# Kernel tuning notes

Measured on AMD Instinct MI355X. Metric: run time of the kernel, lower is better.

## Reference

```python
import jax, jax.numpy as jnp
import numpy as np

B, S, DIM = 4, 2048, 512
HEADS, DHEAD = 8, 64
INNER = HEADS * DHEAD


def setup_inputs() -> dict:
    key = jax.random.key(0)
    k1, k2, k3, k4 = jax.random.split(key, 4)
    x = jax.random.normal(k1, (B, S, DIM), dtype=jnp.float32)
    W_qkv = jax.random.normal(k2, (DIM, 3 * INNER), dtype=jnp.float32) * (DIM ** -0.5)
    W_out = jax.random.normal(k3, (INNER, DIM), dtype=jnp.float32) * (INNER ** -0.5)
    b_out = jnp.zeros((DIM,), dtype=jnp.float32)
    # learnable log-temperature, initialized to log(dim_head**-0.5)
    log_temp = jnp.asarray(np.log(DHEAD ** -0.5), dtype=jnp.float32)
    return {"x": x, "W_qkv": W_qkv, "log_temp": log_temp, "W_out": W_out, "b_out": b_out}


def reference(x, W_qkv, log_temp, W_out, b_out):
    b, s, _ = x.shape
    qkv = x @ W_qkv  # [b, s, 3*inner]
    q, k, v = jnp.split(qkv, 3, axis=-1)
    # [b, s, inner] -> [b, h, s, d]
    reshape = lambda t: t.reshape(b, s, HEADS, DHEAD).transpose(0, 2, 1, 3)
    q, k, v = reshape(q), reshape(k), reshape(v)
    dots = jnp.einsum("bhid,bhjd->bhij", q, k) * jnp.exp(log_temp)
    mask_value = -jnp.finfo(dots.dtype).max
    eye = jnp.eye(s, dtype=bool)
    dots = jnp.where(eye, mask_value, dots)
    attn = jax.nn.softmax(dots, axis=-1)
    out = jnp.einsum("bhij,bhjd->bhid", attn, v)
    out = out.transpose(0, 2, 1, 3).reshape(b, s, INNER)
    return out @ W_out + b_out
```

## Files before the change

kernel.cpp:

```cpp
#include <hip/hip_runtime.h>
#include <hip/hip_bf16.h>

#define BB 4
#define SS 2048
#define DIMM 512
#define HH 8
#define DD 64
#define NQKV 1536

typedef float  floatx4 __attribute__((ext_vector_type(4)));
typedef short  bf16x8  __attribute__((ext_vector_type(8)));
typedef short  bf16x4  __attribute__((ext_vector_type(4)));

#define MFMA16(A, B, C) __builtin_amdgcn_mfma_f32_16x16x32_bf16(A, B, C, 0, 0, 0)

__device__ __forceinline__ unsigned short f2bf(float f) {
    unsigned int u = __float_as_uint(f);
    u += 0x7FFFu + ((u >> 16) & 1u);
    return (unsigned short)(u >> 16);
}

__device__ __forceinline__ unsigned int f2bf_pk(float lo, float hi) {
    float2 f; f.x = lo; f.y = hi;
    __hip_bfloat162 h = __float22bfloat162_rn(f);
    return *reinterpret_cast<unsigned int*>(&h);
}

__device__ __forceinline__ float fast_exp2(float x) {
#if __has_builtin(__builtin_amdgcn_exp2f)
    return __builtin_amdgcn_exp2f(x);
#else
    return __exp2f(x);
#endif
}

__device__ __forceinline__ void gl_lds16(const void* g, void* l) {
    __builtin_amdgcn_global_load_lds(
        (__attribute__((address_space(1))) void*)g,
        (__attribute__((address_space(3))) void*)l,
        16, 0, 0);
}

__global__ __launch_bounds__(256) void k_prep(
    const float* __restrict__ x, const float* __restrict__ W_qkv,
    const float* __restrict__ W_out,
    unsigned short* __restrict__ xb, unsigned short* __restrict__ Wq_t,
    unsigned short* __restrict__ Wo_t) {
    __shared__ float t[32][33];
    int bid = blockIdx.x, tid = threadIdx.x;
    if (bid < 4096) {
        int i = (bid * 256 + tid) * 4;
        float4 v = *(const float4*)(x + i);
        ushort4 o;
        o.x = f2bf(v.x); o.y = f2bf(v.y); o.z = f2bf(v.z); o.w = f2bf(v.w);
        *(ushort4*)(xb + i) = o;
        return;
    }
    const float* in; unsigned short* out; int R = 512, C, bx, by;
    if (bid < 4864) { in = W_qkv; out = Wq_t; C = 1536; int blk = bid - 4096; bx = blk % 48; by = blk / 48; }
    else            { in = W_out; out = Wo_t; C = 512;  int blk = bid - 4864; bx = blk % 16; by = blk / 16; }
    int tx = tid & 31, ty = tid >> 5;
    int c0 = bx * 32, r0 = by * 32;
    for (int i = 0; i < 4; i++) {
        int r = r0 + ty + i * 8;
        t[ty + i * 8][tx] = in[(size_t)r * C + c0 + tx];
    }
    __syncthreads();
    for (int i = 0; i < 4; i++) {
        int cc = c0 + ty + i * 8;
        out[(size_t)cc * R + r0 + tx] = f2bf(t[tx][ty + i * 8]);
    }
}

__global__ __launch_bounds__(256) void k_gemm_qkv(
    const unsigned short* __restrict__ A,
    const unsigned short* __restrict__ Bt,
    const float* __restrict__ log_temp,
    unsigned short* __restrict__ Qb,
    unsigned short* __restrict__ Kb,
    unsigned short* __restrict__ Vt) {
    __shared__ unsigned short smem[2][128 * 64];
    unsigned short* As = smem[0];
    unsigned short* Bs = smem[1];
    const int K = 512;
    int m0 = blockIdx.x * 128, n0 = blockIdx.y * 128;
    int tid = threadIdx.x;
    int w = tid >> 6, lane = tid & 63;
    int c = lane & 15, q4 = lane >> 4;
    int wm = w >> 1, wn = w & 1;
    float qscale = __expf(log_temp[0]) * 1.44269504f;

    floatx4 acc[4][4] = {};

    for (int k0 = 0; k0 < K; k0 += 64) {
        __syncthreads();
        for (int i = 0; i < 4; i++) {
            int cidx = w * 256 + i * 64 + lane;
            int row = cidx >> 3, cc = cidx & 7;
            int gcc = cc ^ (row & 7);
            gl_lds16(A + (size_t)(m0 + row) * K + k0 + gcc * 8,
                     As + (size_t)(w * 256 + i * 64) * 8);
            gl_lds16(Bt + (size_t)(n0 + row) * K + k0 + gcc * 8,
                     Bs + (size_t)(w * 256 + i * 64) * 8);
        }
        __syncthreads();
        bf16x8 aF[2][4], bF[2][4];
        for (int kh = 0; kh < 2; kh++)
            for (int mt = 0; mt < 4; mt++) {
                int row = wm * 64 + mt * 16 + c;
                aF[kh][mt] = *(const bf16x8*)&As[row * 64 + (((kh * 4 + q4) ^ (row & 7)) * 8)];
            }
        for (int kh = 0; kh < 2; kh++)
            for (int nt = 0; nt < 4; nt++) {
                int row = wn * 64 + nt * 16 + c;
                bF[kh][nt] = *(const bf16x8*)&Bs[row * 64 + (((kh * 4 + q4) ^ (row & 7)) * 8)];
            }
        for (int kh = 0; kh < 2; kh++)
            for (int mt = 0; mt < 4; mt++)
                for (int nt = 0; nt < 4; nt++)
                    acc[mt][nt] = MFMA16(aF[kh][mt], bF[kh][nt], acc[mt][nt]);
    }

    if (n0 < 1024) {
        for (int nt = 0; nt < 4; nt++) {
            int n = n0 + wn * 64 + nt * 16 + c;
            int t = n >> 9, inner = n & 511;
            int h = inner >> 6, d = inner & 63;
            for (int mt = 0; mt < 4; mt++) {
                for (int r = 0; r < 4; r++) {
                    int m = m0 + wm * 64 + mt * 16 + q4 * 4 + r;
                    int b = m >> 11, s = m & 2047;
                    int bh = b * 8 + h;
                    float v = acc[mt][nt][r];
                    if (t == 0)  Qb[((size_t)bh * SS + s) * 64 + d] = f2bf(v * qscale);
                    else         Kb[((size_t)bh * SS + s) * 64 + d] = f2bf(v);
                }
            }
        }
    } else {
        unsigned short* T = &smem[0][0];
        int b = m0 >> 11, s_base = m0 & 2047;
        for (int half = 0; half < 2; half++) {
            __syncthreads();
            if (wn == half) {
                for (int nt = 0; nt < 4; nt++)
                    for (int mt = 0; mt < 4; mt++)
                        for (int r = 0; r < 4; r++)
                            T[(nt * 16 + c) * 136 + wm * 64 + mt * 16 + q4 * 4 + r] =
                                f2bf(acc[mt][nt][r]);
            }
            __syncthreads();
            for (int rr = 0; rr < 4; rr++) {
                int nl = w * 16 + rr * 4 + q4;
                int ml = c * 8;
                bf16x8 v = *(const bf16x8*)&T[nl * 136 + ml];
                int n = n0 + half * 64 + nl;
                int h = (n >> 6) - 16, d = n & 63;
                int bh = b * 8 + h;
                *(bf16x8*)(Vt + ((size_t)bh * 64 + d) * SS + s_base + ml) = v;
            }
        }
    }
}

__global__ __launch_bounds__(256, 4) void k_attn(
    const unsigned short* __restrict__ Qb,
    const unsigned short* __restrict__ Kb,
    const unsigned short* __restrict__ Vt,
    unsigned short* __restrict__ AO) {
    __shared__ unsigned short Ks[2][64 * 64];
    __shared__ unsigned short Vs[2][64 * 64];
    int q0 = blockIdx.x * 128;
    int h = blockIdx.y, b = blockIdx.z;
    int bh = b * 8 + h;
    int tid = threadIdx.x, w = tid >> 6, lane = tid & 63;
    int c = lane & 15, q4 = lane >> 4;

    const unsigned short* Kbase = Kb + (size_t)bh * SS * 64;
    const unsigned short* Vbase = Vt + (size_t)bh * 64 * SS;

    bf16x8 qf[2][2];
    for (int mt = 0; mt < 2; mt++) {
        const unsigned short* qp = Qb + ((size_t)bh * SS + q0 + w * 32 + mt * 16 + c) * 64;
        qf[mt][0] = *(const bf16x8*)(qp + q4 * 8);
        qf[mt][1] = *(const bf16x8*)(qp + 32 + q4 * 8);
    }

    int cidx0 = w * 128 + lane, cidx1 = cidx0 + 64;
    int row0 = cidx0 >> 3, cc0 = cidx0 & 7;
    int row1 = cidx1 >> 3, cc1 = cidx1 & 7;
    int fk0 = (row0 & 3) | ((row0 >> 1) & 4);
    int fk1 = (row1 & 3) | ((row1 >> 1) & 4);
    const unsigned short* ksrc0 = Kbase + (size_t)row0 * 64 + (cc0 ^ fk0) * 8;
    const unsigned short* ksrc1 = Kbase + (size_t)row1 * 64 + (cc1 ^ fk1) * 8;
    const unsigned short* vsrc0 = Vbase + (size_t)row0 * SS + (cc0 ^ (row0 & 7)) * 8;
    const unsigned short* vsrc1 = Vbase + (size_t)row1 * SS + (cc1 ^ (row1 & 7)) * 8;
    unsigned short* kdst0 = &Ks[0][0] + w * 1024;
    unsigned short* kdst1 = kdst0 + 512;
    unsigned short* vdst0 = &Vs[0][0] + w * 1024;
    unsigned short* vdst1 = vdst0 + 512;

    gl_lds16(ksrc0, kdst0); gl_lds16(ksrc1, kdst1);
    gl_lds16(vsrc0, vdst0); gl_lds16(vsrc1, vdst1);

    int mask_j0 = (q0 + w * 32) & ~63;
    int mglob0 = q0 + w * 32 + c;
    int mglob1 = mglob0 + 16;
    floatx4 oacc[2][4] = {};
    float psum[2] = {0.f, 0.f};

    for (int j0 = 0; j0 < SS; j0 += 64) {
        int buf = (j0 >> 6) & 1;
        __syncthreads();
        if (j0 + 64 < SS) {
            gl_lds16(ksrc0 + (size_t)(j0 + 64) * 64, kdst0 + (buf ^ 1) * 4096);
            gl_lds16(ksrc1 + (size_t)(j0 + 64) * 64, kdst1 + (buf ^ 1) * 4096);
            gl_lds16(vsrc0 + (j0 + 64), vdst0 + (buf ^ 1) * 4096);
            gl_lds16(vsrc1 + (j0 + 64), vdst1 + (buf ^ 1) * 4096);
        }
        bool diag = (j0 == mask_j0);

        for (int g = 0; g < 2; g++) {
            bf16x8 kf[2][2];
            for (int inner = 0; inner < 2; inner++) {
                int row = g * 32 + ((c >> 2) << 3) + inner * 4 + (c & 3);
                kf[inner][0] = *(const bf16x8*)&Ks[buf][row * 64 + ((q4 ^ (c & 7)) * 8)];
                kf[inner][1] = *(const bf16x8*)&Ks[buf][row * 64 + (((4 + q4) ^ (c & 7)) * 8)];
            }
            bf16x8 vf[4];
            for (int dt = 0; dt < 4; dt++) {
                int vrow = dt * 16 + c;
                vf[dt] = *(const bf16x8*)&Vs[buf][vrow * 64 + (((g * 4 + q4) ^ (c & 7)) * 8)];
            }

            floatx4 sa[2][2];
            for (int mt = 0; mt < 2; mt++)
                for (int inner = 0; inner < 2; inner++) {
                    floatx4 t = {};
                    t = MFMA16(kf[inner][0], qf[mt][0], t);
                    t = MFMA16(kf[inner][1], qf[mt][1], t);
                    sa[mt][inner] = t;
                }

            if (diag) {
                for (int inner = 0; inner < 2; inner++)
                    for (int r = 0; r < 4; r++) {
                        int jg = j0 + g * 32 + q4 * 8 + inner * 4 + r;
                        if (jg == mglob0) sa[0][inner][r] = -1e30f;
                        if (jg == mglob1) sa[1][inner][r] = -1e30f;
                    }
            }

            for (int mt = 0; mt < 2; mt++) {
                float e0 = fast_exp2(sa[mt][0][0]), e1 = fast_exp2(sa[mt][0][1]);
                float e2 = fast_exp2(sa[mt][0][2]), e3 = fast_exp2(sa[mt][0][3]);
                float e4 = fast_exp2(sa[mt][1][0]), e5 = fast_exp2(sa[mt][1][1]);
                float e6 = fast_exp2(sa[mt][1][2]), e7 = fast_exp2(sa[mt][1][3]);
                psum[mt] += ((e0 + e1) + (e2 + e3)) + ((e4 + e5) + (e6 + e7));
                union { bf16x8 v; unsigned int u[4]; } P;
                P.u[0] = f2bf_pk(e0, e1); P.u[1] = f2bf_pk(e2, e3);
                P.u[2] = f2bf_pk(e4, e5); P.u[3] = f2bf_pk(e6, e7);
                for (int dt = 0; dt < 4; dt++)
                    oacc[mt][dt] = MFMA16(P.v, vf[dt], oacc[mt][dt]);
            }
        }
    }

    for (int mt = 0; mt < 2; mt++) {
        float l = psum[mt];
        l += __shfl_xor(l, 16);
        l += __shfl_xor(l, 32);
        for (int r = 0; r < 4; r++) {
            float lr = __shfl(l, q4 * 4 + r, 64);
            float inv = 1.0f / lr;
            int s = q0 + w * 32 + mt * 16 + q4 * 4 + r;
            for (int dt = 0; dt < 4; dt++)
                AO[((size_t)b * SS + s) * 512 + h * 64 + dt * 16 + c] =
                    f2bf(oacc[mt][dt][r] * inv);
        }
    }
}

__global__ __launch_bounds__(256) void k_gemm_out(
    const unsigned short* __restrict__ A,
    const unsigned short* __restrict__ Bt,
    const float* __restrict__ bias,
    float* __restrict__ out) {
    __shared__ unsigned short As[64 * 64];
    __shared__ unsigned short Bs[128 * 64];
    const int K = 512;
    int m0 = blockIdx.x * 64, n0 = blockIdx.y * 128;
    int tid = threadIdx.x;
    int w = tid >> 6, lane = tid & 63;
    int c = lane & 15, q4 = lane >> 4;

    floatx4 acc[8] = {};

    for (int k0 = 0; k0 < K; k0 += 64) {
        __syncthreads();
        for (int i = 0; i < 2; i++) {
            int cidx = i * 256 + tid;
            int row = cidx >> 3, cc = cidx & 7;
            int gcc = cc ^ (row & 7);
            gl_lds16(A + (size_t)(m0 + row) * K + k0 + gcc * 8,
                     As + (size_t)(i * 256 + w * 64) * 8);
        }
        for (int i = 0; i < 4; i++) {
            int cidx = i * 256 + tid;
            int row = cidx >> 3, cc = cidx & 7;
            int gcc = cc ^ (row & 7);
            gl_lds16(Bt + (size_t)(n0 + row) * K + k0 + gcc * 8,
                     Bs + (size_t)(i * 256 + w * 64) * 8);
        }
        __syncthreads();
        bf16x8 aF[2], bF[2][8];
        for (int kh = 0; kh < 2; kh++) {
            int row = w * 16 + c;
            aF[kh] = *(const bf16x8*)&As[row * 64 + (((kh * 4 + q4) ^ (row & 7)) * 8)];
        }
        for (int kh = 0; kh < 2; kh++)
            for (int nt = 0; nt < 8; nt++) {
                int row = nt * 16 + c;
                bF[kh][nt] = *(const bf16x8*)&Bs[row * 64 + (((kh * 4 + q4) ^ (row & 7)) * 8)];
            }
        for (int kh = 0; kh < 2; kh++)
            for (int nt = 0; nt < 8; nt++)
                acc[nt] = MFMA16(aF[kh], bF[kh][nt], acc[nt]);
    }

    for (int nt = 0; nt < 8; nt++) {
        int n = n0 + nt * 16 + c;
        float bv = bias[n];
        for (int r = 0; r < 4; r++) {
            int m = m0 + w * 16 + q4 * 4 + r;
            out[(size_t)m * 512 + n] = acc[nt][r] + bv;
        }
    }
}

extern "C" void kernel_launch(void* const* d_in, const int* in_sizes, int n_in,
                              void* d_out, int out_size, void* d_ws, size_t ws_size,
                              hipStream_t stream) {
    const float* x        = (const float*)d_in[0];
    const float* W_qkv    = (const float*)d_in[1];
    const float* log_temp = (const float*)d_in[2];
    const float* W_out    = (const float*)d_in[3];
    const float* b_out    = (const float*)d_in[4];
    float* out = (float*)d_out;

    char* ws = (char*)d_ws;
    unsigned short* xb   = (unsigned short*)(ws + 0);
    unsigned short* Wq_t = (unsigned short*)(ws + 8388608);
    unsigned short* Wo_t = (unsigned short*)(ws + 9961472);
    unsigned short* Qb   = (unsigned short*)(ws + 10485760);
    unsigned short* Kb   = (unsigned short*)(ws + 18874368);
    unsigned short* Vt   = (unsigned short*)(ws + 27262976);
    unsigned short* AO   = (unsigned short*)(ws + 35651584);

    k_prep<<<5120, 256, 0, stream>>>(x, W_qkv, W_out, xb, Wq_t, Wo_t);
    k_gemm_qkv<<<dim3(64, 12), 256, 0, stream>>>(xb, Wq_t, log_temp, Qb, Kb, Vt);
    k_attn<<<dim3(16, 8, 4), 256, 0, stream>>>(Qb, Kb, Vt, AO);
    k_gemm_out<<<dim3(128, 4), 256, 0, stream>>>(AO, Wo_t, b_out, out);
}
```

Baseline: 156.2 us.

## Split attention key range across two wave groups and reduce partials in LDS

The attention kernel now launches 512 threads per block, split into two groups of four waves. Each group streams half of the key/value sequence with its own double-buffered LDS tiles. The groups then combine partial output accumulators and row sums through shared memory before normalization. This doubles the waves working on each query tile to improve latency hiding and occupancy, at the cost of doubled LDS usage and an extra reduction step.

```diff
diff --git a/kernel.cpp b/kernel.cpp
--- a/kernel.cpp
+++ b/kernel.cpp
@@ -163,74 +163,78 @@
     }
 }
 
-__global__ __launch_bounds__(256, 4) void k_attn(
+__global__ __launch_bounds__(512, 4) void k_attn(
     const unsigned short* __restrict__ Qb,
     const unsigned short* __restrict__ Kb,
     const unsigned short* __restrict__ Vt,
     unsigned short* __restrict__ AO) {
-    __shared__ unsigned short Ks[2][64 * 64];
-    __shared__ unsigned short Vs[2][64 * 64];
+    __shared__ unsigned short KVs[2][2][2][64 * 64];
     int q0 = blockIdx.x * 128;
     int h = blockIdx.y, b = blockIdx.z;
     int bh = b * 8 + h;
     int tid = threadIdx.x, w = tid >> 6, lane = tid & 63;
+    int wg = w >> 2, wi = w & 3;
     int c = lane & 15, q4 = lane >> 4;
 
-    const unsigned short* Kbase = Kb + (size_t)bh * SS * 64;
+    const unsigned short* Kbase = Kb + (size_t)bh * SS * 64 + (size_t)wg * 1024 * 64;
     const unsigned short* Vbase = Vt + (size_t)bh * 64 * SS;
 
     bf16x8 qf[2][2];
     for (int mt = 0; mt < 2; mt++) {
-        const unsigned short* qp = Qb + ((size_t)bh * SS + q0 + w * 32 + mt * 16 + c) * 64;
+        const unsigned short* qp = Qb + ((size_t)bh * SS + q0 + wi * 32 + mt * 16 + c) * 64;
         qf[mt][0] = *(const bf16x8*)(qp + q4 * 8);
         qf[mt][1] = *(const bf16x8*)(qp + 32 + q4 * 8);
     }
 
-    int cidx0 = w * 128 + lane, cidx1 = cidx0 + 64;
+    int cidx0 = wi * 128 + lane, cidx1 = cidx0 + 64;
     int row0 = cidx0 >> 3, cc0 = cidx0 & 7;
     int row1 = cidx1 >> 3, cc1 = cidx1 & 7;
     int fk0 = (row0 & 3) | ((row0 >> 1) & 4);
     int fk1 = (row1 & 3) | ((row1 >> 1) & 4);
     const unsigned short* ksrc0 = Kbase + (size_t)row0 * 64 + (cc0 ^ fk0) * 8;
     const unsigned short* ksrc1 = Kbase + (size_t)row1 * 64 + (cc1 ^ fk1) * 8;
-    const unsigned short* vsrc0 = Vbase + (size_t)row0 * SS + (cc0 ^ (row0 & 7)) * 8;
-    const unsigned short* vsrc1 = Vbase + (size_t)row1 * SS + (cc1 ^ (row1 & 7)) * 8;
-    unsigned short* kdst0 = &Ks[0][0] + w * 1024;
+    const unsigned short* vsrc0 = Vbase + (size_t)row0 * SS + wg * 1024 + (cc0 ^ (row0 & 7)) * 8;
+    const unsigned short* vsrc1 = Vbase + (size_t)row1 * SS + wg * 1024 + (cc1 ^ (row1 & 7)) * 8;
+    unsigned short* kdst0 = &KVs[0][wg][0][0] + wi * 1024;
     unsigned short* kdst1 = kdst0 + 512;
-    unsigned short* vdst0 = &Vs[0][0] + w * 1024;
+    unsigned short* vdst0 = &KVs[1][wg][0][0] + wi * 1024;
     unsigned short* vdst1 = vdst0 + 512;
 
     gl_lds16(ksrc0, kdst0); gl_lds16(ksrc1, kdst1);
     gl_lds16(vsrc0, vdst0); gl_lds16(vsrc1, vdst1);
 
-    int mask_j0 = (q0 + w * 32) & ~63;
-    int mglob0 = q0 + w * 32 + c;
+    int mask_j0 = (q0 + wi * 32) & ~63;
+    int mglob0 = q0 + wi * 32 + c;
     int mglob1 = mglob0 + 16;
     floatx4 oacc[2][4] = {};
     float psum[2] = {0.f, 0.f};
 
-    for (int j0 = 0; j0 < SS; j0 += 64) {
-        int buf = (j0 >> 6) & 1;
-        __syncthreads();
-        if (j0 + 64 < SS) {
-            gl_lds16(ksrc0 + (size_t)(j0 + 64) * 64, kdst0 + (buf ^ 1) * 4096);
-            gl_lds16(ksrc1 + (size_t)(j0 + 64) * 64, kdst1 + (buf ^ 1) * 4096);
-            gl_lds16(vsrc0 + (j0 + 64), vdst0 + (buf ^ 1) * 4096);
-            gl_lds16(vsrc1 + (j0 + 64), vdst1 + (buf ^ 1) * 4096);
+    for (int jt = 0; jt < 16; jt++) {
+        int buf = jt & 1;
+        int j0 = wg * 1024 + jt * 64;
+        __syncthreads();
+        if (jt + 1 < 16) {
+            int jl = (jt + 1) * 64;
+            gl_lds16(ksrc0 + (size_t)jl * 64, kdst0 + (buf ^ 1) * 4096);
+            gl_lds16(ksrc1 + (size_t)jl * 64, kdst1 + (buf ^ 1) * 4096);
+            gl_lds16(vsrc0 + jl, vdst0 + (buf ^ 1) * 4096);
+            gl_lds16(vsrc1 + jl, vdst1 + (buf ^ 1) * 4096);
         }
         bool diag = (j0 == mask_j0);
+        const unsigned short* Ksb = &KVs[0][wg][buf][0];
+        const unsigned short* Vsb = &KVs[1][wg][buf][0];
 
         for (int g = 0; g < 2; g++) {
             bf16x8 kf[2][2];
             for (int inner = 0; inner < 2; inner++) {
                 int row = g * 32 + ((c >> 2) << 3) + inner * 4 + (c & 3);
-                kf[inner][0] = *(const bf16x8*)&Ks[buf][row * 64 + ((q4 ^ (c & 7)) * 8)];
-                kf[inner][1] = *(const bf16x8*)&Ks[buf][row * 64 + (((4 + q4) ^ (c & 7)) * 8)];
+                kf[inner][0] = *(const bf16x8*)&Ksb[row * 64 + ((q4 ^ (c & 7)) * 8)];
+                kf[inner][1] = *(const bf16x8*)&Ksb[row * 64 + (((4 + q4) ^ (c & 7)) * 8)];
             }
             bf16x8 vf[4];
             for (int dt = 0; dt < 4; dt++) {
                 int vrow = dt * 16 + c;
-                vf[dt] = *(const bf16x8*)&Vs[buf][vrow * 64 + (((g * 4 + q4) ^ (c & 7)) * 8)];
+                vf[dt] = *(const bf16x8*)&Vsb[vrow * 64 + (((g * 4 + q4) ^ (c & 7)) * 8)];
             }
 
             floatx4 sa[2][2];
@@ -266,17 +270,35 @@
         }
     }
 
-    for (int mt = 0; mt < 2; mt++) {
-        float l = psum[mt];
-        l += __shfl_xor(l, 16);
-        l += __shfl_xor(l, 32);
-        for (int r = 0; r < 4; r++) {
-            float lr = __shfl(l, q4 * 4 + r, 64);
-            float inv = 1.0f / lr;
-            int s = q0 + w * 32 + mt * 16 + q4 * 4 + r;
+    __syncthreads();
+    float* p = (float*)&KVs[0][0][0][0] + ((size_t)(wi * 64 + lane)) * 35;
+    if (wg == 1) {
+        for (int mt = 0; mt < 2; mt++)
             for (int dt = 0; dt < 4; dt++)
-                AO[((size_t)b * SS + s) * 512 + h * 64 + dt * 16 + c] =
-                    f2bf(oacc[mt][dt][r] * inv);
+                for (int r = 0; r < 4; r++)
+                    p[mt * 16 + dt * 4 + r] = oacc[mt][dt][r];
+        p[32] = psum[0]; p[33] = psum[1];
+    }
+    __syncthreads();
+    if (wg == 0) {
+        for (int mt = 0; mt < 2; mt++)
+            for (int dt = 0; dt < 4; dt++)
+                for (int r = 0; r < 4; r++)
+                    oacc[mt][dt][r] += p[mt * 16 + dt * 4 + r];
+        psum[0] += p[32]; psum[1] += p[33];
+
+        for (int mt = 0; mt < 2; mt++) {
+            float l = psum[mt];
+            l += __shfl_xor(l, 16);
+            l += __shfl_xor(l, 32);
+            for (int r = 0; r < 4; r++) {
+                float lr = __shfl(l, q4 * 4 + r, 64);
+                float inv = 1.0f / lr;
+                int s = q0 + wi * 32 + mt * 16 + q4 * 4 + r;
+                for (int dt = 0; dt < 4; dt++)
+                    AO[((size_t)b * SS + s) * 512 + h * 64 + dt * 16 + c] =
+                        f2bf(oacc[mt][dt][r] * inv);
+            }
         }
     }
 }
@@ -359,6 +381,6 @@
 
     k_prep<<<5120, 256, 0, stream>>>(x, W_qkv, W_out, xb, Wq_t, Wo_t);
     k_gemm_qkv<<<dim3(64, 12), 256, 0, stream>>>(xb, Wq_t, log_temp, Qb, Kb, Vt);
-    k_attn<<<dim3(16, 8, 4), 256, 0, stream>>>(Qb, Kb, Vt, AO);
+    k_attn<<<dim3(16, 8, 4), 512, 0, stream>>>(Qb, Kb, Vt, AO);
     k_gemm_out<<<dim3(128, 4), 256, 0, stream>>>(AO, Wo_t, b_out, out);
 }
```

New measurement: 147.1 us. 5.8% less time.
